# Performance work log

Measured on AMD Instinct MI355X. Metric: run time of the kernel, lower is better.

The kernel has to match this reference:

```python
import jax, jax.numpy as jnp
import numpy as np
from jax import lax

# ---- constants mirroring Prediction.__init__ kwargs ----
INP = 608
NUM_CLASSES = 20
ALPHA, BETA = 1.0, 0.5
OBJ_T, CONF_T, LOC_T = 0.6, 0.05, 0.5
NMS_T, SIZE_T, SIGMA = 0.1, 0.0, 0.5
TOP_K = 8
M_CAND = 256          # fixed-size candidate cap for jit-compatible NMS
NEG = -1e9            # sentinel for masked scores
ANCHORS = [[(116, 90), (156, 198), (373, 326)],
           [(30, 61), (62, 45), (59, 119)],
           [(10, 13), (16, 30), (33, 23)]]


def _decode(pred, anchors):
    """pred: (B, A, G, G, 6+C) raw level output -> decoded flat tensors."""
    B, A, G, _, C = pred.shape
    stride = INP // G
    xy = jax.nn.sigmoid(pred[..., 0:2])
    g = jnp.arange(G, dtype=pred.dtype)
    gx, gy = jnp.meshgrid(g, g)                      # gx[i,j]=j, gy[i,j]=i (np.meshgrid 'xy')
    off = jnp.stack([gx, gy], axis=-1)[None, None]   # (1,1,G,G,2)
    xy = ALPHA * xy - 0.5 * (ALPHA - 1.0) + off
    anc = jnp.asarray(anchors, dtype=pred.dtype) / stride  # (A,2) scaled to grid units
    wh = jnp.exp(pred[..., 2:4]) * anc[None, :, None, None, :]
    box = jnp.concatenate([xy, wh], axis=-1) * stride       # back to pixel units
    obj = jax.nn.sigmoid(pred[..., 4])
    loc = jax.nn.sigmoid(pred[..., 5])
    clsp = jax.nn.softmax(pred[..., 6:], axis=-1)
    N = A * G * G
    return (box.reshape(B, N, 4), obj.reshape(B, N),
            loc.reshape(B, N), clsp.reshape(B, N, NUM_CLASSES))


def _soft_nms(boxes, s0, cls):
    """Per-image Gaussian soft-NMS (class-aware), +1 pixel IoU convention as in bbox_iou.
    boxes: (M,4) xyxy, s0: (M,) scores (NEG for invalid), cls: (M,) int. Returns kept mask."""
    M = s0.shape[0]

    def step(carry, _):
        s, kept = carry
        j = jnp.argmax(s)
        do = s[j] >= NMS_T
        kept = kept | ((jnp.arange(M) == j) & do)
        bj = boxes[j]
        ix1 = jnp.maximum(bj[0], boxes[:, 0]); iy1 = jnp.maximum(bj[1], boxes[:, 1])
        ix2 = jnp.minimum(bj[2], boxes[:, 2]); iy2 = jnp.minimum(bj[3], boxes[:, 3])
        inter = jnp.maximum(ix2 - ix1 + 1.0, 0.0) * jnp.maximum(iy2 - iy1 + 1.0, 0.0)
        a1 = (bj[2] - bj[0] + 1.0) * (bj[3] - bj[1] + 1.0)
        a2 = (boxes[:, 2] - boxes[:, 0] + 1.0) * (boxes[:, 3] - boxes[:, 1] + 1.0)
        iou = inter / (a1 + a2 - inter + 1e-16)
        decay = jnp.exp(-(iou * iou) / SIGMA)
        s_new = jnp.where(cls == cls[j], s * decay, s).at[j].set(NEG)
        s = jnp.where(do, s_new, s)
        return (s, kept), None

    (_, kept), _ = lax.scan(step, (s0, jnp.zeros(M, dtype=bool)), None, length=M)
    return kept


def _forward(pred_l0, pred_l1, pred_l2):
    parts = [_decode(p, a) for p, a in zip([pred_l0, pred_l1, pred_l2], ANCHORS)]
    box = jnp.concatenate([p[0] for p in parts], axis=1)   # (B,N,4) xywh
    obj = jnp.concatenate([p[1] for p in parts], axis=1)
    loc = jnp.concatenate([p[2] for p in parts], axis=1)
    clsp = jnp.concatenate([p[3] for p in parts], axis=1)

    cx, cy, w, h = box[..., 0], box[..., 1], box[..., 2], box[..., 3]
    x1 = jnp.clip(cx - w / 2, 0.0, INP); y1 = jnp.clip(cy - h / 2, 0.0, INP)
    x2 = jnp.clip(cx + w / 2, 0.0, INP); y2 = jnp.clip(cy + h / 2, 0.0, INP)
    boxes = jnp.stack([x1, y1, x2, y2], axis=-1)            # (B,N,4) xyxy, clamped

    cls_conf = jnp.max(clsp, axis=-1)
    cls_id = jnp.argmax(clsp, axis=-1)
    area = (x2 - x1) * (y2 - y1)
    valid = ((obj >= OBJ_T) & (area >= INP * INP * SIZE_T)
             & (obj * cls_conf >= CONF_T) & (loc >= LOC_T))
    score = (obj * cls_conf) ** BETA * loc ** (1.0 - BETA)
    masked = jnp.where(valid, score, NEG)

    # fixed-size candidate set per image (descending-score sort + cap)
    vals, idx = lax.top_k(masked, M_CAND)                   # (B,M)
    cboxes = jnp.take_along_axis(boxes, idx[..., None], axis=1)
    ccls = jnp.take_along_axis(cls_id, idx, axis=1)
    s0 = jnp.where(vals > NEG / 2, vals, NEG)

    kept = jax.vmap(_soft_nms)(cboxes, s0, ccls)            # (B,M) bool

    # keep_top_k: top_k among kept, ranked by ORIGINAL (pre-decay) score
    fscore = jnp.where(kept, vals, NEG)
    fvals, fidx = lax.top_k(fscore, TOP_K)                  # (B,TOP_K)
    fboxes = jnp.take_along_axis(cboxes, fidx[..., None], axis=1)
    fcls = jnp.take_along_axis(ccls, fidx, axis=1)
    row = jnp.concatenate([fboxes, fvals[..., None],
                           fcls[..., None].astype(fboxes.dtype)], axis=-1)  # (B,K,6)
    ok = fvals > NEG / 2
    return jnp.where(ok[..., None], row, 0.0)


def setup_inputs() -> dict:
    key = jax.random.key(0)
    k0, k1, k2 = jax.random.split(key, 3)
    return {
        "pred_l0": jax.random.normal(k0, (64, 3, 19, 19, 26), dtype=jnp.float32),
        "pred_l1": jax.random.normal(k1, (64, 3, 38, 38, 26), dtype=jnp.float32),
        "pred_l2": jax.random.normal(k2, (64, 3, 76, 76, 26), dtype=jnp.float32),
    }


def reference(pred_l0, pred_l1, pred_l2):
    return _forward(pred_l0, pred_l1, pred_l2)
```

## Files before the change

### kernel.cpp

```cpp
#include <hip/hip_runtime.h>
#include <climits>
#include <cstdint>

constexpr int kB  = 64;
constexpr int kG0 = 19, kG1 = 38, kG2 = 76;
constexpr int kN0 = 3 * kG0 * kG0;
constexpr int kN1 = 3 * kG1 * kG1;
constexpr int kN2 = 3 * kG2 * kG2;
constexpr int kN  = kN0 + kN1 + kN2;
constexpr int kNP = kN + 1;
constexpr int kM  = 256;
constexpr int kTopK = 8;
constexpr float kNEG = -1e9f;
constexpr int kHB = 4096;

constexpr int kT0 = 5, kT1 = 17, kT2 = 68;
constexpr int kTilesPerImg = kT0 + kT1 + kT2;
constexpr int kGridScore = 1920;
constexpr int kTilesPerBlk = 3;

__constant__ float c_anchors[3][3][2] = {
    {{116.f, 90.f}, {156.f, 198.f}, {373.f, 326.f}},
    {{30.f, 61.f},  {62.f, 45.f},   {59.f, 119.f}},
    {{10.f, 13.f},  {16.f, 30.f},   {33.f, 23.f}},
};

typedef float f4_t __attribute__((ext_vector_type(4)));

__device__ __forceinline__ float fexpf(float x) { return __expf(x); }
__device__ __forceinline__ float frcpf(float x) { return __builtin_amdgcn_rcpf(x); }
__device__ __forceinline__ float fsigm(float x) { return frcpf(1.0f + __expf(-x)); }

__device__ __forceinline__ float2 nt_load_f2(const float2* p) {
  unsigned long long v = __builtin_nontemporal_load((const unsigned long long*)p);
  union { unsigned long long u; float2 f; } c; c.u = v; return c.f;
}
__device__ __forceinline__ f4_t nt_load_f4(const f4_t* p) {
  return __builtin_nontemporal_load(p);
}

__device__ __forceinline__ unsigned score_to_key(float s) {
  unsigned fb = __float_as_uint(s);
  unsigned m = (fb & 0x80000000u) ? 0xFFFFFFFFu : 0x80000000u;
  return fb ^ m;
}
__device__ __forceinline__ float key_to_score(unsigned k) {
  unsigned fb = (k & 0x80000000u) ? (k ^ 0x80000000u) : ~k;
  return __uint_as_float(fb);
}

__device__ __forceinline__ const float* cell_ptr(
    const float* p0, const float* p1, const float* p2, int b, int n,
    int& lvl, int& a, int& gi, int& gj, float& stride) {
  const float* src; int G, m;
  if (n < kN0)            { src = p0; G = kG0; lvl = 0; m = n;             stride = 32.f; }
  else if (n < kN0 + kN1) { src = p1; G = kG1; lvl = 1; m = n - kN0;       stride = 16.f; }
  else                    { src = p2; G = kG2; lvl = 2; m = n - kN0 - kN1; stride = 8.f; }
  int gg = G * G;
  a = m / gg;
  int r = m - a * gg;
  gi = r / G;
  gj = r - gi * G;
  return src + (size_t)((((b * 3 + a) * G + gi) * G + gj)) * 26;
}

__device__ __forceinline__ void waveArgmax(float& v, int& i) {
  #pragma unroll
  for (int off = 1; off < 64; off <<= 1) {
    float ov = __shfl_xor(v, off);
    int oi = __shfl_xor(i, off);
    if (ov > v || (ov == v && oi < i)) { v = ov; i = oi; }
  }
}
__device__ __forceinline__ float waveMax(float v) {
  #pragma unroll
  for (int off = 1; off < 64; off <<= 1) v = fmaxf(v, __shfl_xor(v, off));
  return v;
}
__device__ __forceinline__ float sel4f(const float a[4], int q) {
  float r = a[0];
  r = (q == 1) ? a[1] : r;
  r = (q == 2) ? a[2] : r;
  r = (q == 3) ? a[3] : r;
  return r;
}
__device__ __forceinline__ int sel4i(const int a[4], int q) {
  int r = a[0];
  r = (q == 1) ? a[1] : r;
  r = (q == 2) ? a[2] : r;
  r = (q == 3) ? a[3] : r;
  return r;
}

__global__ __launch_bounds__(256) void score_kernel(
    const float* __restrict__ p0, const float* __restrict__ p1, const float* __restrict__ p2,
    unsigned* __restrict__ keys, int* __restrict__ gHist)
{
  __shared__ float lds[2][256 * 26];

  int t = threadIdx.x;

  const float* gb[kTilesPerBlk];
  int nc[kTilesPerBlk], nfl[kTilesPerBlk], n0[kTilesPerBlk], bb[kTilesPerBlk];
  bool al16[kTilesPerBlk];
  #pragma unroll
  for (int j = 0; j < kTilesPerBlk; ++j) {
    int tileId = (int)blockIdx.x + j * kGridScore;
    int b = tileId / kTilesPerImg;
    int r = tileId - b * kTilesPerImg;
    const float* slab; int NL, lvlOff, tile;
    if (r < kT0)            { slab = p0; NL = kN0; lvlOff = 0;         tile = r; }
    else if (r < kT0 + kT1) { slab = p1; NL = kN1; lvlOff = kN0;       tile = r - kT0; }
    else                    { slab = p2; NL = kN2; lvlOff = kN0 + kN1; tile = r - kT0 - kT1; }
    int cellBase = tile * 256;
    nc[j]  = min(256, NL - cellBase);
    nfl[j] = nc[j] * 26;
    gb[j]  = slab + ((size_t)b * NL + cellBase) * 26;
    al16[j] = ((((uintptr_t)gb[j]) & 15) == 0);
    n0[j] = lvlOff + cellBase;
    bb[j] = b;
  }

  float sreg[28];

  auto stageLoad = [&](int j) {
    const float* g = gb[j]; int nf = nfl[j];
    if (al16[j]) {
      int n4 = nf >> 2;
      #pragma unroll
      for (int k = 0; k < 7; ++k) {
        int i = t + k * 256;
        if (i < n4) {
          f4_t v = nt_load_f4((const f4_t*)g + i);
          sreg[4*k] = v[0]; sreg[4*k+1] = v[1]; sreg[4*k+2] = v[2]; sreg[4*k+3] = v[3];
        }
      }
      if ((nf & 3) && t == 0) {
        float2 v = nt_load_f2((const float2*)g + (n4 << 1));
        sreg[26] = v.x; sreg[27] = v.y;
      }
    } else {
      int n2 = nf >> 1;
      #pragma unroll
      for (int k = 0; k < 13; ++k) {
        int i = t + k * 256;
        if (i < n2) {
          float2 v = nt_load_f2((const float2*)g + i);
          sreg[2*k] = v.x; sreg[2*k+1] = v.y;
        }
      }
    }
  };
  auto stageWrite = [&](int j, float* dst) {
    int nf = nfl[j];
    if (al16[j]) {
      int n4 = nf >> 2;
      f4_t* d4 = (f4_t*)dst;
      #pragma unroll
      for (int k = 0; k < 7; ++k) {
        int i = t + k * 256;
        if (i < n4) {
          f4_t w; w[0] = sreg[4*k]; w[1] = sreg[4*k+1]; w[2] = sreg[4*k+2]; w[3] = sreg[4*k+3];
          d4[i] = w;
        }
      }
      if ((nf & 3) && t == 0) {
        float2* d2 = (float2*)dst;
        float2 w; w.x = sreg[26]; w.y = sreg[27];
        d2[n4 << 1] = w;
      }
    } else {
      int n2 = nf >> 1;
      float2* d2 = (float2*)dst;
      #pragma unroll
      for (int k = 0; k < 13; ++k) {
        int i = t + k * 256;
        if (i < n2) { float2 w; w.x = sreg[2*k]; w.y = sreg[2*k+1]; d2[i] = w; }
      }
    }
  };

  stageLoad(0);
  stageWrite(0, &lds[0][0]);

  #pragma unroll
  for (int j = 0; j < kTilesPerBlk; ++j) {
    __syncthreads();

    if (j + 1 < kTilesPerBlk) stageLoad(j + 1);

    int curNc = nc[j], curN0 = n0[j], curB = bb[j];
    if (t < curNc) {
      const float2* c2 = (const float2*)&lds[j & 1][t * 26];
      float2 ol = c2[2];
      float obj = fsigm(ol.x);
      float loc = fsigm(ol.y);
      float tch[20];
      #pragma unroll
      for (int q = 0; q < 10; ++q) { float2 v = c2[3 + q]; tch[2*q] = v.x; tch[2*q+1] = v.y; }
      float lm = tch[0];
      #pragma unroll
      for (int c = 1; c < 20; ++c) lm = fmaxf(lm, tch[c]);
      float se = 0.f;
      #pragma unroll
      for (int c = 0; c < 20; ++c) se += fexpf(tch[c] - lm);
      float cls_conf = frcpf(se);
      float conf = obj * cls_conf;
      float masked = (obj >= 0.6f && loc >= 0.5f && conf >= 0.05f)
                     ? sqrtf(conf) * sqrtf(loc) : kNEG;
      unsigned key = score_to_key(masked);
      keys[(size_t)curB * kNP + curN0 + t] = key;
      if (key & 0x80000000u) atomicAdd(&gHist[curB * kHB + (int)(key >> 20)], 1);
    }

    if (j + 1 < kTilesPerBlk) stageWrite(j + 1, &lds[(j + 1) & 1][0]);
  }
}

__device__ __forceinline__ void findThresholdBin(
    const int* hist, int NB, int needed,
    int& outB, int& outCumAbove, int& outTotal,
    int* shWave, int* shOut)
{
  int tid = threadIdx.x, lane = tid & 63, w = tid >> 6;
  if (tid == 0) { shOut[0] = -1; shOut[1] = 0; }
  int ipt = (NB + 511) / 512;
  int base = tid * ipt;
  int csum = 0;
  for (int i = 0; i < ipt; ++i) { int bn = base + i; if (bn < NB) csum += hist[bn]; }
  int v = csum;
  #pragma unroll
  for (int off = 1; off < 64; off <<= 1) {
    int tv = __shfl_down(v, off);
    if (lane + off < 64) v += tv;
  }
  if (lane == 0) shWave[w] = v;
  __syncthreads();
  int above = 0, total = 0;
  #pragma unroll
  for (int q = 0; q < 8; ++q) {
    int wt = shWave[q];
    total += wt;
    if (q > w) above += wt;
  }
  int S = v + above;
  if (S >= needed && S - csum < needed) {
    int running = S - csum;
    for (int i = ipt - 1; i >= 0; --i) {
      int bn = base + i; if (bn >= NB) continue;
      int c = hist[bn];
      if (running + c >= needed) { shOut[0] = bn; shOut[1] = running; break; }
      running += c;
    }
  }
  __syncthreads();
  outB = shOut[0]; outCumAbove = shOut[1]; outTotal = total;
  __syncthreads();
}

constexpr int kNV4 = kN / 4;
constexpr int kTail = kN - kNV4*4;

__global__ __launch_bounds__(512) void select_nms_kernel(
    const unsigned* __restrict__ keys, const int* __restrict__ gHist,
    const float* __restrict__ p0, const float* __restrict__ p1, const float* __restrict__ p2,
    float* __restrict__ out)
{
  int b = blockIdx.x, tid = threadIdx.x;
  const unsigned* kk = keys + (size_t)b * kNP;
  const uint4* kk4 = (const uint4*)kk;
  const unsigned keyNEG = score_to_key(kNEG);

  constexpr int kPool = 4096;
  __shared__ int hist[kHB];
  __shared__ int shWave[8], shOut[2];
  __shared__ int ciL[kM];
  __shared__ unsigned ckL[kM];
  __shared__ unsigned pk[kPool];
  __shared__ int piA[kPool];
  __shared__ int eqI[256];
  __shared__ int sCnt, eqCnt, sTie;

  for (int i = tid; i < kHB; i += 512) hist[i] = gHist[(size_t)b * kHB + i];
  __syncthreads();
  int B, cumAbove1, total1;
  findThresholdBin(hist, kHB, kM, B, cumAbove1, total1, shWave, shOut);

  if (tid == 0) { sCnt = 0; eqCnt = 0; sTie = 0; }
  for (int i = tid; i < kHB; i += 512) hist[i] = 0;
  __syncthreads();

  if (total1 < kM) {
    for (int x = tid; x < kNV4; x += 512) {
      uint4 v = kk4[x];
      int i4 = x * 4;
      unsigned kv[4] = {v.x, v.y, v.z, v.w};
      #pragma unroll
      for (int e = 0; e < 4; ++e) {
        unsigned k = kv[e];
        if (k & 0x80000000u) { int p = atomicAdd(&sCnt, 1); ciL[p] = i4 + e; ckL[p] = k; }
      }
    }
    if (tid < kTail) {
      int x = kNV4 * 4 + tid;
      unsigned k = kk[x];
      if (k & 0x80000000u) { int p = atomicAdd(&sCnt, 1); ciL[p] = x; ckL[p] = k; }
    }
    __syncthreads();
    if (tid >= total1 && tid < kM) { ciL[tid] = -1; ckL[tid] = keyNEG; }
    __syncthreads();
  } else {
    unsigned uB = (unsigned)B;
    for (int x = tid; x < kNV4; x += 512) {
      uint4 v = kk4[x];
      int i4 = x * 4;
      unsigned kv[4] = {v.x, v.y, v.z, v.w};
      #pragma unroll
      for (int e = 0; e < 4; ++e) {
        unsigned k = kv[e];
        unsigned hi = k >> 20;
        if (hi > uB) { int p = atomicAdd(&sCnt, 1); ciL[p] = i4 + e; ckL[p] = k; }
        else if (hi == uB) {
          int p = atomicAdd(&eqCnt, 1);
          if (p < kPool) { pk[p] = k; piA[p] = i4 + e; }
          atomicAdd(&hist[(k >> 8) & 0xFFFu], 1);
        }
      }
    }
    if (tid < kTail) {
      int x = kNV4 * 4 + tid;
      unsigned k = kk[x];
      unsigned hi = k >> 20;
      if (hi > uB) { int p = atomicAdd(&sCnt, 1); ciL[p] = x; ckL[p] = k; }
      else if (hi == uB) {
        int p = atomicAdd(&eqCnt, 1);
        if (p < kPool) { pk[p] = k; piA[p] = x; }
        atomicAdd(&hist[(k >> 8) & 0xFFFu], 1);
      }
    }
    __syncthreads();

    int needed = kM - cumAbove1;
    int pc = eqCnt;

    if (pc == needed) {
      if (tid < pc) { ciL[cumAbove1 + tid] = piA[tid]; ckL[cumAbove1 + tid] = pk[tid]; }
      __syncthreads();
    } else if (pc <= kPool) {
      int B2, cA2, tot2;
      findThresholdBin(hist, kHB, needed, B2, cA2, tot2, shWave, shOut);
      for (int i = tid; i < 256; i += 512) hist[i] = 0;
      __syncthreads();
      for (int i = tid; i < pc; i += 512) {
        unsigned k = pk[i];
        int mid = (int)((k >> 8) & 0xFFFu);
        if (mid > B2) { int p = atomicAdd(&sCnt, 1); ciL[p] = piA[i]; ckL[p] = k; }
        else if (mid == B2) atomicAdd(&hist[k & 0xFFu], 1);
      }
      __syncthreads();
      int needed3 = needed - cA2;
      int B3, cA3, tot3;
      findThresholdBin(hist, 256, needed3, B3, cA3, tot3, shWave, shOut);
      for (int i = tid; i < pc; i += 512) {
        unsigned k = pk[i];
        int mid = (int)((k >> 8) & 0xFFFu);
        if (mid == B2) {
          int lo = (int)(k & 0xFFu);
          if (lo > B3) { int p = atomicAdd(&sCnt, 1); ciL[p] = piA[i]; ckL[p] = k; }
          else if (lo == B3) { int p = atomicAdd(&sTie, 1); if (p < 256) eqI[p] = piA[i]; }
        }
      }
      __syncthreads();
      int needed4 = needed3 - cA3;
      unsigned exactKey = (uB << 20) | ((unsigned)B2 << 8) | (unsigned)B3;
      int nt_ = sTie;
      if (nt_ == needed4) {
        if (tid < needed4) {
          int base0 = kM - needed4;
          ciL[base0 + tid] = eqI[tid]; ckL[base0 + tid] = exactKey;
        }
      } else if (tid == 0) {
        int base0 = kM - needed4; int lastI = -1;
        for (int q = 0; q < needed4; ++q) {
          int mv = INT_MAX;
          for (int x = 0; x < pc; ++x) {
            if (pk[x] == exactKey) { int ix = piA[x]; if (ix > lastI && ix < mv) mv = ix; }
          }
          ciL[base0 + q] = mv; ckL[base0 + q] = exactKey; lastI = mv;
        }
      }
      __syncthreads();
    } else {
      if (tid == 0) {
        int base0 = sCnt;
        unsigned lastK = 0xFFFFFFFFu; int lastI = INT_MAX;
        for (int q = 0; q < needed; ++q) {
          unsigned bk = 0u; int bi2 = -1;
          for (int x = 0; x < kN; ++x) {
            unsigned k = kk[x];
            if ((k >> 20) != uB) continue;
            if (k > lastK || (k == lastK && x <= lastI)) continue;
            if (bi2 < 0 || k > bk || (k == bk && x < bi2)) { bk = k; bi2 = x; }
          }
          ciL[base0 + q] = bi2; ckL[base0 + q] = bk; lastK = bk; lastI = bi2;
        }
      }
      __syncthreads();
    }
  }

  if (tid >= 64) return;
  int lane = tid;

  float x1[4], y1[4], x2[4], y2[4], val[4], s[4];
  int cls[4];
  bool kept[4];

  #pragma unroll
  for (int q = 0; q < 4; ++q) {
    int slot = q * 64 + lane;
    int n = ciL[slot];
    float sc = key_to_score(ckL[slot]);
    kept[q] = false;
    x1[q] = y1[q] = x2[q] = y2[q] = 0.f;
    cls[q] = 0; val[q] = sc; s[q] = sc;
    if (n >= 0) {
      int lvl, a, gi, gj; float stride;
      const float* p = cell_ptr(p0, p1, p2, b, n, lvl, a, gi, gj, stride);
      const float2* r2 = (const float2*)p;
      float2 c01 = r2[0], c23 = r2[1];
      float cx = (fsigm(c01.x) + (float)gj) * stride;
      float cy = (fsigm(c01.y) + (float)gi) * stride;
      float w = fexpf(c23.x) * c_anchors[lvl][a][0];
      float h = fexpf(c23.y) * c_anchors[lvl][a][1];
      x1[q] = fminf(fmaxf(cx - 0.5f * w, 0.f), 608.f);
      y1[q] = fminf(fmaxf(cy - 0.5f * h, 0.f), 608.f);
      x2[q] = fminf(fmaxf(cx + 0.5f * w, 0.f), 608.f);
      y2[q] = fminf(fmaxf(cy + 0.5f * h, 0.f), 608.f);
      float lm = -3.4e38f; int mc = 0;
      #pragma unroll
      for (int j = 3; j < 13; ++j) {
        float2 v = r2[j];
        int c0 = 2 * (j - 3);
        if (v.x > lm) { lm = v.x; mc = c0; }
        if (v.y > lm) { lm = v.y; mc = c0 + 1; }
      }
      cls[q] = mc;
    }
  }

  float top8[8];
  #pragma unroll
  for (int i = 0; i < 8; ++i) top8[i] = kNEG;
  int keptCount = 0;

  for (int it = 0; it < kM; ++it) {
    float bv = s[0]; int bq = 0;
    #pragma unroll
    for (int q = 1; q < 4; ++q) if (s[q] > bv) { bv = s[q]; bq = q; }
    int bi = bq * 64 + lane;
    waveArgmax(bv, bi);
    if (bv < 0.1f) break;

    int wlane = bi & 63, wq = bi >> 6;
    float jx1 = __shfl(sel4f(x1, wq), wlane);
    float jy1 = __shfl(sel4f(y1, wq), wlane);
    float jx2 = __shfl(sel4f(x2, wq), wlane);
    float jy2 = __shfl(sel4f(y2, wq), wlane);
    float jval = __shfl(sel4f(val, wq), wlane);
    int   cj  = __shfl(sel4i(cls, wq), wlane);

    float a1 = (jx2 - jx1 + 1.0f) * (jy2 - jy1 + 1.0f);
    #pragma unroll
    for (int q = 0; q < 4; ++q) {
      if (cls[q] == cj) {
        float ix1 = fmaxf(jx1, x1[q]), iy1 = fmaxf(jy1, y1[q]);
        float ix2 = fminf(jx2, x2[q]), iy2 = fminf(jy2, y2[q]);
        float inter = fmaxf(ix2 - ix1 + 1.0f, 0.0f) * fmaxf(iy2 - iy1 + 1.0f, 0.0f);
        float a2 = (x2[q] - x1[q] + 1.0f) * (y2[q] - y1[q] + 1.0f);
        float iou = inter / (a1 + a2 - inter + 1e-16f);
        s[q] *= fexpf(-(iou * iou) * 2.0f);
      }
      if (bi == q * 64 + lane) { kept[q] = true; s[q] = kNEG; }
    }

    float v = jval;
    #pragma unroll
    for (int i = 0; i < 8; ++i) { float m = fmaxf(top8[i], v); v = fminf(top8[i], v); top8[i] = m; }
    ++keptCount;
    if (keptCount >= kTopK) {
      float am = kNEG;
      #pragma unroll
      for (int q = 0; q < 4; ++q) if (s[q] >= 0.1f) am = fmaxf(am, val[q]);
      am = waveMax(am);
      if (am < top8[7]) break;
    }
  }

  float f[4];
  #pragma unroll
  for (int q = 0; q < 4; ++q) f[q] = kept[q] ? val[q] : kNEG;
  for (int k = 0; k < kTopK; ++k) {
    float bv = f[0]; int bq = 0;
    #pragma unroll
    for (int q = 1; q < 4; ++q) if (f[q] > bv) { bv = f[q]; bq = q; }
    int bi = bq * 64 + lane;
    waveArgmax(bv, bi);
    int wlane = bi & 63, wq = bi >> 6;
    if (lane == wlane) {
      float* o = out + (size_t)(b * kTopK + k) * 6;
      if (bv > kNEG * 0.5f) {
        o[0] = sel4f(x1, wq); o[1] = sel4f(y1, wq);
        o[2] = sel4f(x2, wq); o[3] = sel4f(y2, wq);
        o[4] = sel4f(val, wq); o[5] = (float)sel4i(cls, wq);
      } else {
        o[0] = 0.f; o[1] = 0.f; o[2] = 0.f; o[3] = 0.f; o[4] = 0.f; o[5] = 0.f;
      }
    }
    #pragma unroll
    for (int q = 0; q < 4; ++q) if (bi == q * 64 + lane) f[q] = kNEG;
  }
}

extern "C" void kernel_launch(void* const* d_in, const int* in_sizes, int n_in,
                              void* d_out, int out_size, void* d_ws, size_t ws_size,
                              hipStream_t stream) {
  const float* p0 = (const float*)d_in[0];
  const float* p1 = (const float*)d_in[1];
  const float* p2 = (const float*)d_in[2];
  float* out = (float*)d_out;

  unsigned* keys = (unsigned*)d_ws;
  int* gHist = (int*)((char*)d_ws + (size_t)kB * kNP * sizeof(unsigned));

  hipMemsetAsync(gHist, 0, (size_t)kB * kHB * sizeof(int), stream);
  score_kernel<<<kGridScore, 256, 0, stream>>>(p0, p1, p2, keys, gHist);
  select_nms_kernel<<<kB, 512, 0, stream>>>(keys, gHist, p0, p1, p2, out);
}
```

Before: 261.3 us.

## Move score histogram into select kernel and drop score-kernel pipelining

The score kernel drops its global histogram atomics and the memset that cleared them, and each block now handles one tile with a single LDS buffer instead of three tiles with register double-buffering. The select kernel builds each image's histogram in shared memory by scanning that image's keys with LDS atomics. This removes a memset launch and contended global atomics, but adds a full pass over the keys (about 22.7K per image) inside the select kernel, which runs only 64 blocks, and gives up the load/compute overlap in the score kernel.

```diff
diff --git a/kernel.cpp b/kernel.cpp
--- a/kernel.cpp
+++ b/kernel.cpp
@@ -16,8 +16,7 @@
 
 constexpr int kT0 = 5, kT1 = 17, kT2 = 68;
 constexpr int kTilesPerImg = kT0 + kT1 + kT2;
-constexpr int kGridScore = 1920;
-constexpr int kTilesPerBlk = 3;
+constexpr int kGridScore = kB * kTilesPerImg;
 
 __constant__ float c_anchors[3][3][2] = {
     {{116.f, 90.f}, {156.f, 198.f}, {373.f, 326.f}},
@@ -94,126 +93,64 @@
 
 __global__ __launch_bounds__(256) void score_kernel(
     const float* __restrict__ p0, const float* __restrict__ p1, const float* __restrict__ p2,
-    unsigned* __restrict__ keys, int* __restrict__ gHist)
+    unsigned* __restrict__ keys)
 {
-  __shared__ float lds[2][256 * 26];
+  __shared__ float lds[256 * 26];
 
   int t = threadIdx.x;
-
-  const float* gb[kTilesPerBlk];
-  int nc[kTilesPerBlk], nfl[kTilesPerBlk], n0[kTilesPerBlk], bb[kTilesPerBlk];
-  bool al16[kTilesPerBlk];
-  #pragma unroll
-  for (int j = 0; j < kTilesPerBlk; ++j) {
-    int tileId = (int)blockIdx.x + j * kGridScore;
-    int b = tileId / kTilesPerImg;
-    int r = tileId - b * kTilesPerImg;
-    const float* slab; int NL, lvlOff, tile;
-    if (r < kT0)            { slab = p0; NL = kN0; lvlOff = 0;         tile = r; }
-    else if (r < kT0 + kT1) { slab = p1; NL = kN1; lvlOff = kN0;       tile = r - kT0; }
-    else                    { slab = p2; NL = kN2; lvlOff = kN0 + kN1; tile = r - kT0 - kT1; }
-    int cellBase = tile * 256;
-    nc[j]  = min(256, NL - cellBase);
-    nfl[j] = nc[j] * 26;
-    gb[j]  = slab + ((size_t)b * NL + cellBase) * 26;
-    al16[j] = ((((uintptr_t)gb[j]) & 15) == 0);
-    n0[j] = lvlOff + cellBase;
-    bb[j] = b;
-  }
-
-  float sreg[28];
-
-  auto stageLoad = [&](int j) {
-    const float* g = gb[j]; int nf = nfl[j];
-    if (al16[j]) {
-      int n4 = nf >> 2;
-      #pragma unroll
-      for (int k = 0; k < 7; ++k) {
-        int i = t + k * 256;
-        if (i < n4) {
-          f4_t v = nt_load_f4((const f4_t*)g + i);
-          sreg[4*k] = v[0]; sreg[4*k+1] = v[1]; sreg[4*k+2] = v[2]; sreg[4*k+3] = v[3];
-        }
-      }
-      if ((nf & 3) && t == 0) {
-        float2 v = nt_load_f2((const float2*)g + (n4 << 1));
-        sreg[26] = v.x; sreg[27] = v.y;
-      }
-    } else {
-      int n2 = nf >> 1;
-      #pragma unroll
-      for (int k = 0; k < 13; ++k) {
-        int i = t + k * 256;
-        if (i < n2) {
-          float2 v = nt_load_f2((const float2*)g + i);
-          sreg[2*k] = v.x; sreg[2*k+1] = v.y;
-        }
-      }
-    }
-  };
-  auto stageWrite = [&](int j, float* dst) {
-    int nf = nfl[j];
-    if (al16[j]) {
-      int n4 = nf >> 2;
-      f4_t* d4 = (f4_t*)dst;
-      #pragma unroll
-      for (int k = 0; k < 7; ++k) {
-        int i = t + k * 256;
-        if (i < n4) {
-          f4_t w; w[0] = sreg[4*k]; w[1] = sreg[4*k+1]; w[2] = sreg[4*k+2]; w[3] = sreg[4*k+3];
-          d4[i] = w;
-        }
-      }
-      if ((nf & 3) && t == 0) {
-        float2* d2 = (float2*)dst;
-        float2 w; w.x = sreg[26]; w.y = sreg[27];
-        d2[n4 << 1] = w;
-      }
-    } else {
-      int n2 = nf >> 1;
-      float2* d2 = (float2*)dst;
-      #pragma unroll
-      for (int k = 0; k < 13; ++k) {
-        int i = t + k * 256;
-        if (i < n2) { float2 w; w.x = sreg[2*k]; w.y = sreg[2*k+1]; d2[i] = w; }
-      }
-    }
-  };
-
-  stageLoad(0);
-  stageWrite(0, &lds[0][0]);
-
-  #pragma unroll
-  for (int j = 0; j < kTilesPerBlk; ++j) {
-    __syncthreads();
-
-    if (j + 1 < kTilesPerBlk) stageLoad(j + 1);
-
-    int curNc = nc[j], curN0 = n0[j], curB = bb[j];
-    if (t < curNc) {
-      const float2* c2 = (const float2*)&lds[j & 1][t * 26];
-      float2 ol = c2[2];
-      float obj = fsigm(ol.x);
-      float loc = fsigm(ol.y);
-      float tch[20];
-      #pragma unroll
-      for (int q = 0; q < 10; ++q) { float2 v = c2[3 + q]; tch[2*q] = v.x; tch[2*q+1] = v.y; }
-      float lm = tch[0];
-      #pragma unroll
-      for (int c = 1; c < 20; ++c) lm = fmaxf(lm, tch[c]);
-      float se = 0.f;
-      #pragma unroll
-      for (int c = 0; c < 20; ++c) se += fexpf(tch[c] - lm);
-      float cls_conf = frcpf(se);
-      float conf = obj * cls_conf;
-      float masked = (obj >= 0.6f && loc >= 0.5f && conf >= 0.05f)
-                     ? sqrtf(conf) * sqrtf(loc) : kNEG;
-      unsigned key = score_to_key(masked);
-      keys[(size_t)curB * kNP + curN0 + t] = key;
-      if (key & 0x80000000u) atomicAdd(&gHist[curB * kHB + (int)(key >> 20)], 1);
-    }
-
-    if (j + 1 < kTilesPerBlk) stageWrite(j + 1, &lds[(j + 1) & 1][0]);
+  int tileId = (int)blockIdx.x;
+  int b = tileId / kTilesPerImg;
+  int r = tileId - b * kTilesPerImg;
+  const float* slab; int NL, lvlOff, tile;
+  if (r < kT0)            { slab = p0; NL = kN0; lvlOff = 0;         tile = r; }
+  else if (r < kT0 + kT1) { slab = p1; NL = kN1; lvlOff = kN0;       tile = r - kT0; }
+  else                    { slab = p2; NL = kN2; lvlOff = kN0 + kN1; tile = r - kT0 - kT1; }
+  int cellBase = tile * 256;
+  int nc = min(256, NL - cellBase);
+  const float* g = slab + ((size_t)b * NL + cellBase) * 26;
+  int nf = nc * 26;
+
+  if ((((uintptr_t)g) & 15) == 0) {
+    int n4 = nf >> 2;
+    f4_t* d4 = (f4_t*)lds;
+    #pragma unroll
+    for (int k = 0; k < 7; ++k) {
+      int i = t + k * 256;
+      if (i < n4) d4[i] = nt_load_f4((const f4_t*)g + i);
+    }
+    if ((nf & 3) && t == 0) {
+      ((float2*)lds)[n4 << 1] = nt_load_f2((const float2*)g + (n4 << 1));
+    }
+  } else {
+    int n2 = nf >> 1;
+    float2* d2 = (float2*)lds;
+    #pragma unroll
+    for (int k = 0; k < 13; ++k) {
+      int i = t + k * 256;
+      if (i < n2) d2[i] = nt_load_f2((const float2*)g + i);
+    }
+  }
+  __syncthreads();
+
+  if (t < nc) {
+    const float2* c2 = (const float2*)&lds[t * 26];
+    float2 ol = c2[2];
+    float obj = fsigm(ol.x);
+    float loc = fsigm(ol.y);
+    float tch[20];
+    #pragma unroll
+    for (int q = 0; q < 10; ++q) { float2 v = c2[3 + q]; tch[2*q] = v.x; tch[2*q+1] = v.y; }
+    float lm = tch[0];
+    #pragma unroll
+    for (int c = 1; c < 20; ++c) lm = fmaxf(lm, tch[c]);
+    float se = 0.f;
+    #pragma unroll
+    for (int c = 0; c < 20; ++c) se += fexpf(tch[c] - lm);
+    float cls_conf = frcpf(se);
+    float conf = obj * cls_conf;
+    float masked = (obj >= 0.6f && loc >= 0.5f && conf >= 0.05f)
+                   ? sqrtf(conf) * sqrtf(loc) : kNEG;
+    keys[(size_t)b * kNP + lvlOff + cellBase + t] = score_to_key(masked);
   }
 }
 
@@ -262,7 +199,7 @@
 constexpr int kTail = kN - kNV4*4;
 
 __global__ __launch_bounds__(512) void select_nms_kernel(
-    const unsigned* __restrict__ keys, const int* __restrict__ gHist,
+    const unsigned* __restrict__ keys,
     const float* __restrict__ p0, const float* __restrict__ p1, const float* __restrict__ p2,
     float* __restrict__ out)
 {
@@ -281,7 +218,19 @@
   __shared__ int eqI[256];
   __shared__ int sCnt, eqCnt, sTie;
 
-  for (int i = tid; i < kHB; i += 512) hist[i] = gHist[(size_t)b * kHB + i];
+  for (int i = tid; i < kHB; i += 512) hist[i] = 0;
+  __syncthreads();
+  for (int x = tid; x < kNV4; x += 512) {
+    uint4 v = kk4[x];
+    if (v.x >= 0x80000000u) atomicAdd(&hist[v.x >> 20], 1);
+    if (v.y >= 0x80000000u) atomicAdd(&hist[v.y >> 20], 1);
+    if (v.z >= 0x80000000u) atomicAdd(&hist[v.z >> 20], 1);
+    if (v.w >= 0x80000000u) atomicAdd(&hist[v.w >> 20], 1);
+  }
+  if (tid < kTail) {
+    unsigned k = kk[kNV4 * 4 + tid];
+    if (k >= 0x80000000u) atomicAdd(&hist[k >> 20], 1);
+  }
   __syncthreads();
   int B, cumAbove1, total1;
   findThresholdBin(hist, kHB, kM, B, cumAbove1, total1, shWave, shOut);
@@ -531,9 +480,7 @@
   float* out = (float*)d_out;
 
   unsigned* keys = (unsigned*)d_ws;
-  int* gHist = (int*)((char*)d_ws + (size_t)kB * kNP * sizeof(unsigned));
-
-  hipMemsetAsync(gHist, 0, (size_t)kB * kHB * sizeof(int), stream);
-  score_kernel<<<kGridScore, 256, 0, stream>>>(p0, p1, p2, keys, gHist);
-  select_nms_kernel<<<kB, 512, 0, stream>>>(keys, gHist, p0, p1, p2, out);
-}
+
+  score_kernel<<<kGridScore, 256, 0, stream>>>(p0, p1, p2, keys);
+  select_nms_kernel<<<kB, 512, 0, stream>>>(keys, p0, p1, p2, out);
+}
```

Measured after the change: 224.2 us. 14.2% less time.
